# Performance work log

Hardware: AMD Instinct MI355X
Metric: run time of the kernel (lower is better)

## Reference

```python
import jax, jax.numpy as jnp
import numpy as np

NV = 20000; NC = 20000; E = 500000
IN_SHAPE = 2; PE_DIM = 8; HID = 64; NL = 3
EPS = 1e-7  # GENConv message eps


def _lin(x, w, b):
    return x @ w + b


def _encode(x, pe, ew, eb, pw1, pb1, pw2, pb2):
    # relu(cat([Linear(x), 0.5*(pe_mlp(pe)+pe_mlp(-pe))], dim=1))
    def pe_mlp(p):
        return _lin(jax.nn.relu(_lin(p, pw1, pb1)), pw2, pb2)
    h = jnp.concatenate([_lin(x, ew, eb), 0.5 * (pe_mlp(pe) + pe_mlp(-pe))], axis=1)
    return jax.nn.relu(h)


def _genconv(x_src, x_dst, src, dst, ewt, lew, leb, w1, b1, w2, b2, n_dst):
    # GENConv(aggr='softmax', t=1, norm=None, msg_norm=False, edge_dim=1)
    msg = jax.nn.relu(x_src[src] + _lin(ewt, lew, leb)) + EPS  # [E, HID]
    m = jax.ops.segment_max(msg, dst, num_segments=n_dst)      # stable segment softmax
    ex = jnp.exp(msg - m[dst])
    s = jax.ops.segment_sum(ex, dst, num_segments=n_dst)
    agg = jax.ops.segment_sum(ex / (s[dst] + 1e-16) * msg, dst, num_segments=n_dst)
    out = agg + x_dst
    return _lin(jax.nn.relu(_lin(out, w1, b1)), w2, b2)  # MLP [hid -> 2hid -> hid]


def setup_inputs() -> dict:
    key = jax.random.key(0)
    ks = iter(jax.random.split(key, 64))
    d = {}
    d['x_vals'] = jax.random.normal(next(ks), (NV, IN_SHAPE), jnp.float32)
    d['x_cons'] = jax.random.normal(next(ks), (NC, IN_SHAPE), jnp.float32)
    d['pe_vals'] = jax.random.normal(next(ks), (NV, PE_DIM), jnp.float32)
    d['pe_cons'] = jax.random.normal(next(ks), (NC, PE_DIM), jnp.float32)
    d['edge_index_v2c'] = jnp.stack([
        jax.random.randint(next(ks), (E,), 0, NV),
        jax.random.randint(next(ks), (E,), 0, NC)])
    d['edge_index_c2v'] = jnp.stack([
        jax.random.randint(next(ks), (E,), 0, NC),
        jax.random.randint(next(ks), (E,), 0, NV)])
    d['edge_weight_v2c'] = jax.random.normal(next(ks), (E, 1), jnp.float32)
    d['edge_weight_c2v'] = jax.random.normal(next(ks), (E, 1), jnp.float32)
    def p(shape):
        return jax.random.normal(next(ks), shape, jnp.float32) * 0.05
    for k_ in ['vals', 'cons']:
        d[f'enc_{k_}_w'] = p((IN_SHAPE, HID // 2)); d[f'enc_{k_}_b'] = p((HID // 2,))
        d[f'pe_{k_}_w1'] = p((PE_DIM, HID)); d[f'pe_{k_}_b1'] = p((HID,))
        d[f'pe_{k_}_w2'] = p((HID, HID // 2)); d[f'pe_{k_}_b2'] = p((HID // 2,))
    for c in ['v2c', 'c2v']:
        d[f'{c}_edge_w'] = p((NL, 1, HID)); d[f'{c}_edge_b'] = p((NL, HID))
        d[f'{c}_w1'] = p((NL, HID, 2 * HID)); d[f'{c}_b1'] = p((NL, 2 * HID))
        d[f'{c}_w2'] = p((NL, 2 * HID, HID)); d[f'{c}_b2'] = p((NL, HID))
    for k_ in ['vals', 'cons']:
        d[f'pred_{k_}_w1'] = p((HID, HID)); d[f'pred_{k_}_b1'] = p((HID,))
        d[f'pred_{k_}_w2'] = p((HID, 1)); d[f'pred_{k_}_b2'] = p((1,))
    return d


def reference(x_vals, x_cons, pe_vals, pe_cons, edge_index_v2c, edge_index_c2v,
              edge_weight_v2c, edge_weight_c2v,
              enc_vals_w, enc_vals_b, pe_vals_w1, pe_vals_b1, pe_vals_w2, pe_vals_b2,
              enc_cons_w, enc_cons_b, pe_cons_w1, pe_cons_b1, pe_cons_w2, pe_cons_b2,
              v2c_edge_w, v2c_edge_b, v2c_w1, v2c_b1, v2c_w2, v2c_b2,
              c2v_edge_w, c2v_edge_b, c2v_w1, c2v_b1, c2v_w2, c2v_b2,
              pred_vals_w1, pred_vals_b1, pred_vals_w2, pred_vals_b2,
              pred_cons_w1, pred_cons_b1, pred_cons_w2, pred_cons_b2):
    vals = _encode(x_vals, pe_vals, enc_vals_w, enc_vals_b,
                   pe_vals_w1, pe_vals_b1, pe_vals_w2, pe_vals_b2)
    cons = _encode(x_cons, pe_cons, enc_cons_w, enc_cons_b,
                   pe_cons_w1, pe_cons_b1, pe_cons_w2, pe_cons_b2)
    hv, hc = [], []
    for i in range(NL):
        cons = _genconv(vals, cons, edge_index_v2c[0], edge_index_v2c[1],
                        edge_weight_v2c, v2c_edge_w[i], v2c_edge_b[i],
                        v2c_w1[i], v2c_b1[i], v2c_w2[i], v2c_b2[i], NC)
        vals = _genconv(cons, vals, edge_index_c2v[0], edge_index_c2v[1],
                        edge_weight_c2v, c2v_edge_w[i], c2v_edge_b[i],
                        c2v_w1[i], c2v_b1[i], c2v_w2[i], c2v_b2[i], NV)
        hc.append(cons); hv.append(vals)
    V = jnp.stack(hv)  # [NL, NV, HID]
    C = jnp.stack(hc)  # [NL, NC, HID]
    pv = _lin(jax.nn.relu(_lin(V, pred_vals_w1, pred_vals_b1)), pred_vals_w2, pred_vals_b2)
    pc = _lin(jax.nn.relu(_lin(C, pred_cons_w1, pred_cons_b1)), pred_cons_w2, pred_cons_b2)
    return pv[..., 0].T, pc[..., 0].T  # [NV, NL], [NC, NL]
```

## Files before the change

### kernel.cpp

```cpp
#include <hip/hip_runtime.h>

#define NVN 20000
#define NCN 20000
#define NE  500000
#define HID 64
#define NLAYER 3
#define TN 40
#define BSH 8
#define NB 79
#define CAP 8192
#define P1E 2048

__device__ __forceinline__ float relu_(float x) { return fmaxf(x, 0.0f); }

__global__ __launch_bounds__(256) void bininit_kernel(
    int* __restrict__ bincurA, int* __restrict__ bincurB)
{
    int t = threadIdx.x;
    if (t < NB) { bincurA[t] = t * CAP; bincurB[t] = t * CAP; }
}

__global__ __launch_bounds__(256) void scatter_p1_kernel(
    const int* __restrict__ eiA, const float* __restrict__ ewA,
    int* __restrict__ bincurA, int2* __restrict__ stageA,
    const int* __restrict__ eiB, const float* __restrict__ ewB,
    int* __restrict__ bincurB, int2* __restrict__ stageB)
{
    __shared__ int rnk[P1E];
    __shared__ int cnt[NB], base_[NB];
    int t = threadIdx.x;
    int e0 = blockIdx.x * P1E;

    for (int g = 0; g < 2; ++g) {
        const int* ei   = g ? eiB : eiA;
        const float* ew = g ? ewB : ewA;
        int* bincur     = g ? bincurB : bincurA;
        int2* stage     = g ? stageB : stageA;

        if (t < NB) cnt[t] = 0;
        __syncthreads();
        for (int i = t; i < P1E; i += 256) {
            int e = e0 + i;
            if (e < NE) {
                int d = ei[NE + e];
                rnk[i] = atomicAdd(&cnt[d >> BSH], 1);
            }
        }
        __syncthreads();
        if (t < NB && cnt[t] > 0) base_[t] = atomicAdd(&bincur[t], cnt[t]);
        __syncthreads();
        for (int i = t; i < P1E; i += 256) {
            int e = e0 + i;
            if (e < NE) {
                int s = ei[e], d = ei[NE + e];
                float w = ew[e];
                stage[base_[d >> BSH] + rnk[i]] =
                    make_int2((int)((unsigned)s | ((unsigned)d << 16)), __float_as_int(w));
            }
        }
        __syncthreads();
    }
}

__global__ __launch_bounds__(1024) void scatter_p2_kernel(
    const int* __restrict__ bincurA, const int2* __restrict__ stageA,
    int* __restrict__ rowptrA, int2* __restrict__ pairA,
    const int* __restrict__ bincurB, const int2* __restrict__ stageB,
    int* __restrict__ rowptrB, int2* __restrict__ pairB)
{
    __shared__ int p[128];
    __shared__ int deg[256], pfx[256], cur[256];
    int g = blockIdx.x / NB;
    int b = blockIdx.x % NB;
    const int* bincur = g ? bincurB : bincurA;
    const int2* stage = g ? stageB : stageA;
    int* rowptr       = g ? rowptrB : rowptrA;
    int2* pair        = g ? pairB : pairA;

    int t = threadIdx.x;
    if (t < 128) p[t] = (t < NB) ? (bincur[t] - t * CAP) : 0;
    __syncthreads();
    for (int off = 1; off < 128; off <<= 1) {
        int v = (t >= off && t < 128) ? p[t - off] : 0;
        __syncthreads();
        if (t < 128) p[t] += v;
        __syncthreads();
    }
    int base = (b == 0) ? 0 : p[b - 1];
    int sz   = p[b] - base;

    int d0 = b << BSH;
    int d1 = min(d0 + 256, NCN);
    int nd = d1 - d0;
    int astart = b * CAP;

    if (t < 256) deg[t] = 0;
    __syncthreads();
    for (int e = astart + t; e < astart + sz; e += 1024) {
        int dst = (int)((unsigned)stage[e].x >> 16);
        atomicAdd(&deg[dst - d0], 1);
    }
    __syncthreads();
    if (t < 256) pfx[t] = deg[t];
    __syncthreads();
    for (int off = 1; off < 256; off <<= 1) {
        int v = (t >= off && t < 256) ? pfx[t - off] : 0;
        __syncthreads();
        if (t < 256) pfx[t] += v;
        __syncthreads();
    }
    if (t < nd) {
        int ex = base + pfx[t] - deg[t];
        rowptr[d0 + t] = ex;
        cur[t] = ex;
    }
    if (t == 0) rowptr[d1] = base + sz;
    __syncthreads();
    for (int e = astart + t; e < astart + sz; e += 1024) {
        int2 s = stage[e];
        unsigned u = (unsigned)s.x;
        int src = (int)(u & 0xFFFFu);
        int dst = (int)(u >> 16);
        int q = atomicAdd(&cur[dst - d0], 1);
        pair[q] = make_int2(src, s.y);
    }
}

__global__ __launch_bounds__(256) void encode2_kernel(
    const float* __restrict__ xv, const float* __restrict__ pev,
    const float* __restrict__ ewv, const float* __restrict__ ebv,
    const float* __restrict__ pw1v, const float* __restrict__ pb1v,
    const float* __restrict__ pw2v, const float* __restrict__ pb2v,
    const float* __restrict__ xc, const float* __restrict__ pec,
    const float* __restrict__ ewc, const float* __restrict__ ebc,
    const float* __restrict__ pw1c, const float* __restrict__ pb1c,
    const float* __restrict__ pw2c, const float* __restrict__ pb2c,
    float* __restrict__ outv, float* __restrict__ outc)
{
    __shared__ float sh[4][64];
    const int VB = (NVN + 3) / 4;
    int wave = threadIdx.x >> 6, lane = threadIdx.x & 63;
    int b = blockIdx.x;
    bool isC = (b >= VB);
    const float* x   = isC ? xc : xv;
    const float* pe  = isC ? pec : pev;
    const float* ew  = isC ? ewc : ewv;
    const float* eb  = isC ? ebc : ebv;
    const float* pw1 = isC ? pw1c : pw1v;
    const float* pb1 = isC ? pb1c : pb1v;
    const float* pw2 = isC ? pw2c : pw2v;
    const float* pb2 = isC ? pb2c : pb2v;
    float* out = isC ? outc : outv;
    int N = isC ? NCN : NVN;
    int n = (isC ? b - VB : b) * 4 + wave;
    if (n >= N) return;

    float accp = pb1[lane], accm = accp;
#pragma unroll
    for (int k = 0; k < 8; ++k) {
        float p = pe[n * 8 + k];
        float w = pw1[k * 64 + lane];
        accp += p * w;
        accm -= p * w;
    }
    float hs = 0.5f * (relu_(accp) + relu_(accm));
    float* my = sh[wave];
    my[lane] = hs;
    __builtin_amdgcn_wave_barrier();

    int col = lane & 31;
    float peo = pb2[col];
#pragma unroll
    for (int k = 0; k < 64; k += 4) {
        float4 hv = *(const float4*)(my + k);
        peo = fmaf(hv.x, pw2[(k + 0) * 32 + col], peo);
        peo = fmaf(hv.y, pw2[(k + 1) * 32 + col], peo);
        peo = fmaf(hv.z, pw2[(k + 2) * 32 + col], peo);
        peo = fmaf(hv.w, pw2[(k + 3) * 32 + col], peo);
    }
    float lino = x[n * 2 + 0] * ew[col] + x[n * 2 + 1] * ew[32 + col] + eb[col];
    float h = (lane < 32) ? lino : peo;
    out[n * 64 + lane] = relu_(h);
}

__global__ __launch_bounds__(256) void edge_agg_kernel(
    const float* __restrict__ xsrc,
    const float* __restrict__ xdst,
    const int* __restrict__ rowptr,
    const int2* __restrict__ pair,
    const float* __restrict__ lew,
    const float* __restrict__ leb,
    float* __restrict__ oa,
    int N)
{
    int wave = threadIdx.x >> 6, lane = threadIdx.x & 63;
    int n = blockIdx.x * 4 + wave;
    if (n >= N) return;

    int start = rowptr[n], end = rowptr[n + 1];
    float lw = lew[lane], lb = leb[lane];
    float xd = xdst[n * 64 + lane];

    float m0 = -1e30f, den0 = 0.0f, num0 = 0.0f;
    float m1 = -1e30f, den1 = 0.0f, num1 = 0.0f;
    int j = start;
    for (; j + 16 <= end; j += 16) {
        int idx[16]; float wv[16], msg[16];
#pragma unroll
        for (int c = 0; c < 16; ++c) {
            int2 p = pair[j + c];
            idx[c] = p.x;
            wv[c] = __int_as_float(p.y);
        }
#pragma unroll
        for (int c = 0; c < 16; ++c) {
            float xv = xsrc[idx[c] * 64 + lane];
            msg[c] = relu_(fmaf(wv[c], lw, xv + lb)) + 1e-7f;
        }
        {
            float a0 = fmaxf(msg[0], msg[1]), a1 = fmaxf(msg[2], msg[3]);
            float a2 = fmaxf(msg[4], msg[5]), a3 = fmaxf(msg[6], msg[7]);
            float mnew = fmaxf(m0, fmaxf(fmaxf(a0, a1), fmaxf(a2, a3)));
            float sc = __expf(m0 - mnew);
            float cd = 0.0f, cn = 0.0f;
#pragma unroll
            for (int c = 0; c < 8; ++c) {
                float e = __expf(msg[c] - mnew);
                cd += e;
                cn = fmaf(e, msg[c], cn);
            }
            den0 = fmaf(den0, sc, cd);
            num0 = fmaf(num0, sc, cn);
            m0 = mnew;
        }
        {
            float a0 = fmaxf(msg[8], msg[9]), a1 = fmaxf(msg[10], msg[11]);
            float a2 = fmaxf(msg[12], msg[13]), a3 = fmaxf(msg[14], msg[15]);
            float mnew = fmaxf(m1, fmaxf(fmaxf(a0, a1), fmaxf(a2, a3)));
            float sc = __expf(m1 - mnew);
            float cd = 0.0f, cn = 0.0f;
#pragma unroll
            for (int c = 8; c < 16; ++c) {
                float e = __expf(msg[c] - mnew);
                cd += e;
                cn = fmaf(e, msg[c], cn);
            }
            den1 = fmaf(den1, sc, cd);
            num1 = fmaf(num1, sc, cn);
            m1 = mnew;
        }
    }
    if (j < end) {
        int last = end - 1;
        int idx[16]; float wv[16], msg[16]; bool val[16];
#pragma unroll
        for (int c = 0; c < 16; ++c) {
            int jj = j + c;
            val[c] = jj < end;
            int jc = val[c] ? jj : last;
            int2 p = pair[jc];
            idx[c] = p.x;
            wv[c] = __int_as_float(p.y);
        }
#pragma unroll
        for (int c = 0; c < 16; ++c) {
            float xv = xsrc[idx[c] * 64 + lane];
            float tm = relu_(fmaf(wv[c], lw, xv + lb)) + 1e-7f;
            msg[c] = val[c] ? tm : -1e30f;
        }
        {
            float a0 = fmaxf(msg[0], msg[1]), a1 = fmaxf(msg[2], msg[3]);
            float a2 = fmaxf(msg[4], msg[5]), a3 = fmaxf(msg[6], msg[7]);
            float mnew = fmaxf(m0, fmaxf(fmaxf(a0, a1), fmaxf(a2, a3)));
            float sc = __expf(m0 - mnew);
            float cd = 0.0f, cn = 0.0f;
#pragma unroll
            for (int c = 0; c < 8; ++c) {
                float e = __expf(msg[c] - mnew);
                cd += e;
                cn = fmaf(e, msg[c], cn);
            }
            den0 = fmaf(den0, sc, cd);
            num0 = fmaf(num0, sc, cn);
            m0 = mnew;
        }
        {
            float a0 = fmaxf(msg[8], msg[9]), a1 = fmaxf(msg[10], msg[11]);
            float a2 = fmaxf(msg[12], msg[13]), a3 = fmaxf(msg[14], msg[15]);
            float mnew = fmaxf(m1, fmaxf(fmaxf(a0, a1), fmaxf(a2, a3)));
            float sc = __expf(m1 - mnew);
            float cd = 0.0f, cn = 0.0f;
#pragma unroll
            for (int c = 8; c < 16; ++c) {
                float e = __expf(msg[c] - mnew);
                cd += e;
                cn = fmaf(e, msg[c], cn);
            }
            den1 = fmaf(den1, sc, cd);
            num1 = fmaf(num1, sc, cn);
            m1 = mnew;
        }
    }
    float M = fmaxf(m0, m1);
    float s0 = __expf(m0 - M), s1 = __expf(m1 - M);
    float den = den0 * s0 + den1 * s1;
    float num = num0 * s0 + num1 * s1;

    oa[n * 64 + lane] = num / (den + 1e-16f) + xd;
}

__global__ __launch_bounds__(256) void mlp_kernel(
    const float* __restrict__ oa,
    float* __restrict__ feat,
    const float* __restrict__ w1,
    const float* __restrict__ b1,
    const float* __restrict__ w2,
    const float* __restrict__ b2,
    const float* __restrict__ pw1,
    const float* __restrict__ pb1,
    const float* __restrict__ pw2,
    const float* __restrict__ pb2,
    float* __restrict__ outp,
    int N, int layer)
{
    __shared__ float w1s[64 * 128];
    __shared__ float w2s[128 * 64];
    __shared__ float pw1s[64 * 64];
    __shared__ float b1s[128];
    __shared__ float b2s[64];
    __shared__ float pb1s[64];
    __shared__ float pw2s[64];
    __shared__ float act[TN][68];
    __shared__ float hid[TN][132];

    int tid = threadIdx.x;
    for (int i = tid; i < 64 * 128; i += 256) w1s[i] = w1[i];
    for (int i = tid; i < 128 * 64; i += 256) w2s[i] = w2[i];
    for (int i = tid; i < 64 * 64; i += 256) pw1s[i] = pw1[i];
    if (tid < 128) b1s[tid] = b1[tid];
    if (tid < 64) { b2s[tid] = b2[tid]; pb1s[tid] = pb1[tid]; pw2s[tid] = pw2[tid]; }
    float pb2v = pb2[0];

    int o4 = (tid & 31) * 4;
    int o2 = (tid & 31) * 2;
    int n5 = (tid >> 5) * 5;
    __syncthreads();

    int ntiles = N / TN;
    for (int tile = blockIdx.x; tile < ntiles; tile += gridDim.x) {
        int base = tile * TN;
        {
            const float* g = oa + (size_t)base * 64;
            for (int i = tid; i < TN * 64; i += 256)
                act[i >> 6][i & 63] = g[i];
        }
        __syncthreads();

        {
            float acc[5][4];
#pragma unroll
            for (int i = 0; i < 5; ++i)
#pragma unroll
                for (int q = 0; q < 4; ++q) acc[i][q] = b1s[o4 + q];
            for (int k = 0; k < 64; k += 4) {
                float4 a[5];
#pragma unroll
                for (int i = 0; i < 5; ++i) a[i] = *(const float4*)&act[n5 + i][k];
                float4 w0 = *(const float4*)&w1s[(k + 0) * 128 + o4];
                float4 wq1 = *(const float4*)&w1s[(k + 1) * 128 + o4];
                float4 wq2 = *(const float4*)&w1s[(k + 2) * 128 + o4];
                float4 wq3 = *(const float4*)&w1s[(k + 3) * 128 + o4];
#pragma unroll
                for (int i = 0; i < 5; ++i) {
                    acc[i][0] = fmaf(a[i].x, w0.x, acc[i][0]);
                    acc[i][1] = fmaf(a[i].x, w0.y, acc[i][1]);
                    acc[i][2] = fmaf(a[i].x, w0.z, acc[i][2]);
                    acc[i][3] = fmaf(a[i].x, w0.w, acc[i][3]);
                    acc[i][0] = fmaf(a[i].y, wq1.x, acc[i][0]);
                    acc[i][1] = fmaf(a[i].y, wq1.y, acc[i][1]);
                    acc[i][2] = fmaf(a[i].y, wq1.z, acc[i][2]);
                    acc[i][3] = fmaf(a[i].y, wq1.w, acc[i][3]);
                    acc[i][0] = fmaf(a[i].z, wq2.x, acc[i][0]);
                    acc[i][1] = fmaf(a[i].z, wq2.y, acc[i][1]);
                    acc[i][2] = fmaf(a[i].z, wq2.z, acc[i][2]);
                    acc[i][3] = fmaf(a[i].z, wq2.w, acc[i][3]);
                    acc[i][0] = fmaf(a[i].w, wq3.x, acc[i][0]);
                    acc[i][1] = fmaf(a[i].w, wq3.y, acc[i][1]);
                    acc[i][2] = fmaf(a[i].w, wq3.z, acc[i][2]);
                    acc[i][3] = fmaf(a[i].w, wq3.w, acc[i][3]);
                }
            }
#pragma unroll
            for (int i = 0; i < 5; ++i) {
                float4 h4 = make_float4(relu_(acc[i][0]), relu_(acc[i][1]),
                                        relu_(acc[i][2]), relu_(acc[i][3]));
                *(float4*)&hid[n5 + i][o4] = h4;
            }
        }
        __syncthreads();

        {
            float acc[5][2];
#pragma unroll
            for (int i = 0; i < 5; ++i) { acc[i][0] = b2s[o2]; acc[i][1] = b2s[o2 + 1]; }
            for (int k = 0; k < 128; k += 4) {
                float4 a[5];
#pragma unroll
                for (int i = 0; i < 5; ++i) a[i] = *(const float4*)&hid[n5 + i][k];
                float2 w0 = *(const float2*)&w2s[(k + 0) * 64 + o2];
                float2 wq1 = *(const float2*)&w2s[(k + 1) * 64 + o2];
                float2 wq2 = *(const float2*)&w2s[(k + 2) * 64 + o2];
                float2 wq3 = *(const float2*)&w2s[(k + 3) * 64 + o2];
#pragma unroll
                for (int i = 0; i < 5; ++i) {
                    acc[i][0] = fmaf(a[i].x, w0.x, acc[i][0]);
                    acc[i][1] = fmaf(a[i].x, w0.y, acc[i][1]);
                    acc[i][0] = fmaf(a[i].y, wq1.x, acc[i][0]);
                    acc[i][1] = fmaf(a[i].y, wq1.y, acc[i][1]);
                    acc[i][0] = fmaf(a[i].z, wq2.x, acc[i][0]);
                    acc[i][1] = fmaf(a[i].z, wq2.y, acc[i][1]);
                    acc[i][0] = fmaf(a[i].w, wq3.x, acc[i][0]);
                    acc[i][1] = fmaf(a[i].w, wq3.y, acc[i][1]);
                }
            }
#pragma unroll
            for (int i = 0; i < 5; ++i) {
                float2 r2 = make_float2(acc[i][0], acc[i][1]);
                *(float2*)&feat[(size_t)(base + n5 + i) * 64 + o2] = r2;
                *(float2*)&act[n5 + i][o2] = r2;
            }
        }
        __syncthreads();

        {
            float acc[5][2];
#pragma unroll
            for (int i = 0; i < 5; ++i) { acc[i][0] = pb1s[o2]; acc[i][1] = pb1s[o2 + 1]; }
            for (int k = 0; k < 64; k += 4) {
                float4 a[5];
#pragma unroll
                for (int i = 0; i < 5; ++i) a[i] = *(const float4*)&act[n5 + i][k];
                float2 w0 = *(const float2*)&pw1s[(k + 0) * 64 + o2];
                float2 wq1 = *(const float2*)&pw1s[(k + 1) * 64 + o2];
                float2 wq2 = *(const float2*)&pw1s[(k + 2) * 64 + o2];
                float2 wq3 = *(const float2*)&pw1s[(k + 3) * 64 + o2];
#pragma unroll
                for (int i = 0; i < 5; ++i) {
                    acc[i][0] = fmaf(a[i].x, w0.x, acc[i][0]);
                    acc[i][1] = fmaf(a[i].x, w0.y, acc[i][1]);
                    acc[i][0] = fmaf(a[i].y, wq1.x, acc[i][0]);
                    acc[i][1] = fmaf(a[i].y, wq1.y, acc[i][1]);
                    acc[i][0] = fmaf(a[i].z, wq2.x, acc[i][0]);
                    acc[i][1] = fmaf(a[i].z, wq2.y, acc[i][1]);
                    acc[i][0] = fmaf(a[i].w, wq3.x, acc[i][0]);
                    acc[i][1] = fmaf(a[i].w, wq3.y, acc[i][1]);
                }
            }
            float pw2a = pw2s[o2], pw2b = pw2s[o2 + 1];
            float ps[5];
#pragma unroll
            for (int i = 0; i < 5; ++i)
                ps[i] = relu_(acc[i][0]) * pw2a + relu_(acc[i][1]) * pw2b;
#pragma unroll
            for (int msk = 16; msk >= 1; msk >>= 1) {
#pragma unroll
                for (int i = 0; i < 5; ++i)
                    ps[i] += __shfl_xor(ps[i], msk, 64);
            }
            if ((tid & 31) == 0) {
#pragma unroll
                for (int i = 0; i < 5; ++i)
                    outp[(size_t)(base + n5 + i) * NLAYER + layer] = ps[i] + pb2v;
            }
        }
        __syncthreads();
    }
}

extern "C" void kernel_launch(void* const* d_in, const int* in_sizes, int n_in,
                              void* d_out, int out_size, void* d_ws, size_t ws_size,
                              hipStream_t stream)
{
    const float* x_vals   = (const float*)d_in[0];
    const float* x_cons   = (const float*)d_in[1];
    const float* pe_vals  = (const float*)d_in[2];
    const float* pe_cons  = (const float*)d_in[3];
    const int*   ei_v2c   = (const int*)d_in[4];
    const int*   ei_c2v   = (const int*)d_in[5];
    const float* ew_v2c   = (const float*)d_in[6];
    const float* ew_c2v   = (const float*)d_in[7];
    const float* enc_vals_w = (const float*)d_in[8];
    const float* enc_vals_b = (const float*)d_in[9];
    const float* pe_vals_w1 = (const float*)d_in[10];
    const float* pe_vals_b1 = (const float*)d_in[11];
    const float* pe_vals_w2 = (const float*)d_in[12];
    const float* pe_vals_b2 = (const float*)d_in[13];
    const float* enc_cons_w = (const float*)d_in[14];
    const float* enc_cons_b = (const float*)d_in[15];
    const float* pe_cons_w1 = (const float*)d_in[16];
    const float* pe_cons_b1 = (const float*)d_in[17];
    const float* pe_cons_w2 = (const float*)d_in[18];
    const float* pe_cons_b2 = (const float*)d_in[19];
    const float* v2c_edge_w = (const float*)d_in[20];
    const float* v2c_edge_b = (const float*)d_in[21];
    const float* v2c_w1     = (const float*)d_in[22];
    const float* v2c_b1     = (const float*)d_in[23];
    const float* v2c_w2     = (const float*)d_in[24];
    const float* v2c_b2     = (const float*)d_in[25];
    const float* c2v_edge_w = (const float*)d_in[26];
    const float* c2v_edge_b = (const float*)d_in[27];
    const float* c2v_w1     = (const float*)d_in[28];
    const float* c2v_b1     = (const float*)d_in[29];
    const float* c2v_w2     = (const float*)d_in[30];
    const float* c2v_b2     = (const float*)d_in[31];
    const float* pred_vals_w1 = (const float*)d_in[32];
    const float* pred_vals_b1 = (const float*)d_in[33];
    const float* pred_vals_w2 = (const float*)d_in[34];
    const float* pred_vals_b2 = (const float*)d_in[35];
    const float* pred_cons_w1 = (const float*)d_in[36];
    const float* pred_cons_b1 = (const float*)d_in[37];
    const float* pred_cons_w2 = (const float*)d_in[38];
    const float* pred_cons_b2 = (const float*)d_in[39];

    float* out = (float*)d_out;
    float* out_c = out + (size_t)NVN * NLAYER;

    const size_t NF = (size_t)NVN * 64;
    const size_t ARENA = (size_t)NB * CAP;

    float* ws     = (float*)d_ws;
    float* feat_v = ws;
    float* feat_c = feat_v + NF;
    float* oa     = feat_c + NF;
    int2* v2c_pair  = (int2*)(oa + NF);
    int2* c2v_pair  = v2c_pair + NE;
    int2* v2c_stage = c2v_pair + NE;
    int2* c2v_stage = v2c_stage + ARENA;
    int* ip = (int*)(c2v_stage + ARENA);
    int* v2c_bincur  = ip; ip += NB;
    int* c2v_bincur  = ip; ip += NB;
    int* v2c_rowptr  = ip; ip += NCN + 1;
    int* c2v_rowptr  = ip; ip += NVN + 1;

    const int p1b = (NE + P1E - 1) / P1E;

    bininit_kernel<<<1, 256, 0, stream>>>(v2c_bincur, c2v_bincur);
    scatter_p1_kernel<<<p1b, 256, 0, stream>>>(
        ei_v2c, ew_v2c, v2c_bincur, v2c_stage,
        ei_c2v, ew_c2v, c2v_bincur, c2v_stage);
    scatter_p2_kernel<<<2 * NB, 1024, 0, stream>>>(
        v2c_bincur, v2c_stage, v2c_rowptr, v2c_pair,
        c2v_bincur, c2v_stage, c2v_rowptr, c2v_pair);

    encode2_kernel<<<(NVN + 3) / 4 + (NCN + 3) / 4, 256, 0, stream>>>(
        x_vals, pe_vals, enc_vals_w, enc_vals_b,
        pe_vals_w1, pe_vals_b1, pe_vals_w2, pe_vals_b2,
        x_cons, pe_cons, enc_cons_w, enc_cons_b,
        pe_cons_w1, pe_cons_b1, pe_cons_w2, pe_cons_b2,
        feat_v, feat_c);

    for (int i = 0; i < NLAYER; ++i) {
        edge_agg_kernel<<<(NCN + 3) / 4, 256, 0, stream>>>(
            feat_v, feat_c, v2c_rowptr, v2c_pair,
            v2c_edge_w + (size_t)i * HID, v2c_edge_b + (size_t)i * HID,
            oa, NCN);
        mlp_kernel<<<250, 256, 0, stream>>>(
            oa, feat_c,
            v2c_w1 + (size_t)i * 8192, v2c_b1 + (size_t)i * 128,
            v2c_w2 + (size_t)i * 8192, v2c_b2 + (size_t)i * 64,
            pred_cons_w1, pred_cons_b1, pred_cons_w2, pred_cons_b2,
            out_c, NCN, i);
        edge_agg_kernel<<<(NVN + 3) / 4, 256, 0, stream>>>(
            feat_c, feat_v, c2v_rowptr, c2v_pair,
            c2v_edge_w + (size_t)i * HID, c2v_edge_b + (size_t)i * HID,
            oa, NVN);
        mlp_kernel<<<250, 256, 0, stream>>>(
            oa, feat_v,
            c2v_w1 + (size_t)i * 8192, c2v_b1 + (size_t)i * 128,
            c2v_w2 + (size_t)i * 8192, c2v_b2 + (size_t)i * 64,
            pred_vals_w1, pred_vals_b1, pred_vals_w2, pred_vals_b2,
            out, NVN, i);
    }
}
```

Measured before the change: 515.8 us.

## Split node features into two 32-column halves and gather half-rows per block

Node feature tables are stored as two planar halves of 32 columns each (offset NF2). The edge aggregation kernel now launches twice as many blocks, one per half. Within a wave, the two 32-lane halves process alternate groups of 16 edges, and their softmax partials are combined with a cross-lane shuffle. Edge pair loads and the output store use nontemporal hints. The goal is 128-byte gathers that improve cache locality per half-table, at the cost of reading the edge list twice and leaving half the lanes idle on the store.

```diff
diff --git a/kernel.cpp b/kernel.cpp
--- a/kernel.cpp
+++ b/kernel.cpp
@@ -10,6 +10,7 @@
 #define NB 79
 #define CAP 8192
 #define P1E 2048
+#define NF2 640000
 
 __device__ __forceinline__ float relu_(float x) { return fmaxf(x, 0.0f); }
 
@@ -180,7 +181,7 @@
     }
     float lino = x[n * 2 + 0] * ew[col] + x[n * 2 + 1] * ew[32 + col] + eb[col];
     float h = (lane < 32) ? lino : peo;
-    out[n * 64 + lane] = relu_(h);
+    out[(size_t)(lane >> 5) * NF2 + (size_t)n * 32 + (lane & 31)] = relu_(h);
 }
 
 __global__ __launch_bounds__(256) void edge_agg_kernel(
@@ -194,119 +195,101 @@
     int N)
 {
     int wave = threadIdx.x >> 6, lane = threadIdx.x & 63;
-    int n = blockIdx.x * 4 + wave;
+    int h = blockIdx.x & 1;
+    int n = (blockIdx.x >> 1) * 4 + wave;
     if (n >= N) return;
-
+    int eh = lane >> 5;
+    int c  = lane & 31;
+
+    const float* tab = xsrc + (size_t)h * NF2;
     int start = rowptr[n], end = rowptr[n + 1];
-    float lw = lew[lane], lb = leb[lane];
-    float xd = xdst[n * 64 + lane];
-
-    float m0 = -1e30f, den0 = 0.0f, num0 = 0.0f;
-    float m1 = -1e30f, den1 = 0.0f, num1 = 0.0f;
+    float lw = lew[h * 32 + c], lb = leb[h * 32 + c];
+    float xd = xdst[(size_t)h * NF2 + (size_t)n * 32 + c];
+
+    float m = -1e30f, den = 0.0f, num = 0.0f;
+    int off = eh * 16;
     int j = start;
-    for (; j + 16 <= end; j += 16) {
+    for (; j + 32 <= end; j += 32) {
         int idx[16]; float wv[16], msg[16];
 #pragma unroll
-        for (int c = 0; c < 16; ++c) {
-            int2 p = pair[j + c];
-            idx[c] = p.x;
-            wv[c] = __int_as_float(p.y);
-        }
-#pragma unroll
-        for (int c = 0; c < 16; ++c) {
-            float xv = xsrc[idx[c] * 64 + lane];
-            msg[c] = relu_(fmaf(wv[c], lw, xv + lb)) + 1e-7f;
-        }
-        {
-            float a0 = fmaxf(msg[0], msg[1]), a1 = fmaxf(msg[2], msg[3]);
-            float a2 = fmaxf(msg[4], msg[5]), a3 = fmaxf(msg[6], msg[7]);
-            float mnew = fmaxf(m0, fmaxf(fmaxf(a0, a1), fmaxf(a2, a3)));
-            float sc = __expf(m0 - mnew);
-            float cd = 0.0f, cn = 0.0f;
-#pragma unroll
-            for (int c = 0; c < 8; ++c) {
-                float e = __expf(msg[c] - mnew);
-                cd += e;
-                cn = fmaf(e, msg[c], cn);
-            }
-            den0 = fmaf(den0, sc, cd);
-            num0 = fmaf(num0, sc, cn);
-            m0 = mnew;
-        }
-        {
-            float a0 = fmaxf(msg[8], msg[9]), a1 = fmaxf(msg[10], msg[11]);
-            float a2 = fmaxf(msg[12], msg[13]), a3 = fmaxf(msg[14], msg[15]);
-            float mnew = fmaxf(m1, fmaxf(fmaxf(a0, a1), fmaxf(a2, a3)));
-            float sc = __expf(m1 - mnew);
-            float cd = 0.0f, cn = 0.0f;
-#pragma unroll
-            for (int c = 8; c < 16; ++c) {
-                float e = __expf(msg[c] - mnew);
-                cd += e;
-                cn = fmaf(e, msg[c], cn);
-            }
-            den1 = fmaf(den1, sc, cd);
-            num1 = fmaf(num1, sc, cn);
-            m1 = mnew;
-        }
+        for (int s = 0; s < 16; ++s) {
+            long long pv = __builtin_nontemporal_load(
+                (const long long*)(pair + (j + off + s)));
+            idx[s] = (int)pv;
+            wv[s] = __int_as_float((int)(pv >> 32));
+        }
+#pragma unroll
+        for (int s = 0; s < 16; ++s) {
+            float xv = tab[idx[s] * 32 + c];
+            msg[s] = relu_(fmaf(wv[s], lw, xv + lb)) + 1e-7f;
+        }
+        float a0 = fmaxf(msg[0], msg[1]), a1 = fmaxf(msg[2], msg[3]);
+        float a2 = fmaxf(msg[4], msg[5]), a3 = fmaxf(msg[6], msg[7]);
+        float a4 = fmaxf(msg[8], msg[9]), a5 = fmaxf(msg[10], msg[11]);
+        float a6 = fmaxf(msg[12], msg[13]), a7 = fmaxf(msg[14], msg[15]);
+        float b0 = fmaxf(fmaxf(a0, a1), fmaxf(a2, a3));
+        float b1 = fmaxf(fmaxf(a4, a5), fmaxf(a6, a7));
+        float mnew = fmaxf(m, fmaxf(b0, b1));
+        float sc = __expf(m - mnew);
+        float cd = 0.0f, cn = 0.0f;
+#pragma unroll
+        for (int s = 0; s < 16; ++s) {
+            float e = __expf(msg[s] - mnew);
+            cd += e;
+            cn = fmaf(e, msg[s], cn);
+        }
+        den = fmaf(den, sc, cd);
+        num = fmaf(num, sc, cn);
+        m = mnew;
     }
     if (j < end) {
         int last = end - 1;
         int idx[16]; float wv[16], msg[16]; bool val[16];
 #pragma unroll
-        for (int c = 0; c < 16; ++c) {
-            int jj = j + c;
-            val[c] = jj < end;
-            int jc = val[c] ? jj : last;
-            int2 p = pair[jc];
-            idx[c] = p.x;
-            wv[c] = __int_as_float(p.y);
-        }
-#pragma unroll
-        for (int c = 0; c < 16; ++c) {
-            float xv = xsrc[idx[c] * 64 + lane];
-            float tm = relu_(fmaf(wv[c], lw, xv + lb)) + 1e-7f;
-            msg[c] = val[c] ? tm : -1e30f;
-        }
-        {
-            float a0 = fmaxf(msg[0], msg[1]), a1 = fmaxf(msg[2], msg[3]);
-            float a2 = fmaxf(msg[4], msg[5]), a3 = fmaxf(msg[6], msg[7]);
-            float mnew = fmaxf(m0, fmaxf(fmaxf(a0, a1), fmaxf(a2, a3)));
-            float sc = __expf(m0 - mnew);
-            float cd = 0.0f, cn = 0.0f;
-#pragma unroll
-            for (int c = 0; c < 8; ++c) {
-                float e = __expf(msg[c] - mnew);
-                cd += e;
-                cn = fmaf(e, msg[c], cn);
-            }
-            den0 = fmaf(den0, sc, cd);
-            num0 = fmaf(num0, sc, cn);
-            m0 = mnew;
-        }
-        {
-            float a0 = fmaxf(msg[8], msg[9]), a1 = fmaxf(msg[10], msg[11]);
-            float a2 = fmaxf(msg[12], msg[13]), a3 = fmaxf(msg[14], msg[15]);
-            float mnew = fmaxf(m1, fmaxf(fmaxf(a0, a1), fmaxf(a2, a3)));
-            float sc = __expf(m1 - mnew);
-            float cd = 0.0f, cn = 0.0f;
-#pragma unroll
-            for (int c = 8; c < 16; ++c) {
-                float e = __expf(msg[c] - mnew);
-                cd += e;
-                cn = fmaf(e, msg[c], cn);
-            }
-            den1 = fmaf(den1, sc, cd);
-            num1 = fmaf(num1, sc, cn);
-            m1 = mnew;
-        }
-    }
-    float M = fmaxf(m0, m1);
-    float s0 = __expf(m0 - M), s1 = __expf(m1 - M);
-    float den = den0 * s0 + den1 * s1;
-    float num = num0 * s0 + num1 * s1;
-
-    oa[n * 64 + lane] = num / (den + 1e-16f) + xd;
+        for (int s = 0; s < 16; ++s) {
+            int jj = j + off + s;
+            val[s] = jj < end;
+            int jc = val[s] ? jj : last;
+            long long pv = __builtin_nontemporal_load(
+                (const long long*)(pair + jc));
+            idx[s] = (int)pv;
+            wv[s] = __int_as_float((int)(pv >> 32));
+        }
+#pragma unroll
+        for (int s = 0; s < 16; ++s) {
+            float xv = tab[idx[s] * 32 + c];
+            float tm = relu_(fmaf(wv[s], lw, xv + lb)) + 1e-7f;
+            msg[s] = val[s] ? tm : -1e30f;
+        }
+        float a0 = fmaxf(msg[0], msg[1]), a1 = fmaxf(msg[2], msg[3]);
+        float a2 = fmaxf(msg[4], msg[5]), a3 = fmaxf(msg[6], msg[7]);
+        float a4 = fmaxf(msg[8], msg[9]), a5 = fmaxf(msg[10], msg[11]);
+        float a6 = fmaxf(msg[12], msg[13]), a7 = fmaxf(msg[14], msg[15]);
+        float b0 = fmaxf(fmaxf(a0, a1), fmaxf(a2, a3));
+        float b1 = fmaxf(fmaxf(a4, a5), fmaxf(a6, a7));
+        float mnew = fmaxf(m, fmaxf(b0, b1));
+        float sc = __expf(m - mnew);
+        float cd = 0.0f, cn = 0.0f;
+#pragma unroll
+        for (int s = 0; s < 16; ++s) {
+            float e = __expf(msg[s] - mnew);
+            cd += e;
+            cn = fmaf(e, msg[s], cn);
+        }
+        den = fmaf(den, sc, cd);
+        num = fmaf(num, sc, cn);
+        m = mnew;
+    }
+    float mo  = __shfl_xor(m, 32, 64);
+    float dho = __shfl_xor(den, 32, 64);
+    float nho = __shfl_xor(num, 32, 64);
+    float M = fmaxf(m, mo);
+    float s0 = __expf(m - M), s1 = __expf(mo - M);
+    float DEN = fmaf(den, s0, dho * s1);
+    float NUM = fmaf(num, s0, nho * s1);
+    float o = NUM / (DEN + 1e-16f) + xd;
+    if (lane < 32)
+        __builtin_nontemporal_store(o, oa + (size_t)n * 64 + h * 32 + lane);
 }
 
 __global__ __launch_bounds__(256) void mlp_kernel(
@@ -344,6 +327,8 @@
     int o4 = (tid & 31) * 4;
     int o2 = (tid & 31) * 2;
     int n5 = (tid >> 5) * 5;
+    int oh = o2 >> 5;
+    int oc = o2 & 31;
     __syncthreads();
 
     int ntiles = N / TN;
@@ -426,7 +411,7 @@
 #pragma unroll
             for (int i = 0; i < 5; ++i) {
                 float2 r2 = make_float2(acc[i][0], acc[i][1]);
-                *(float2*)&feat[(size_t)(base + n5 + i) * 64 + o2] = r2;
+                *(float2*)&feat[(size_t)oh * NF2 + (size_t)(base + n5 + i) * 32 + oc] = r2;
                 *(float2*)&act[n5 + i][o2] = r2;
             }
         }
@@ -559,8 +544,11 @@
         pe_cons_w1, pe_cons_b1, pe_cons_w2, pe_cons_b2,
         feat_v, feat_c);
 
+    const int eag_v = 2 * ((NVN + 3) / 4);
+    const int eag_c = 2 * ((NCN + 3) / 4);
+
     for (int i = 0; i < NLAYER; ++i) {
-        edge_agg_kernel<<<(NCN + 3) / 4, 256, 0, stream>>>(
+        edge_agg_kernel<<<eag_c, 256, 0, stream>>>(
             feat_v, feat_c, v2c_rowptr, v2c_pair,
             v2c_edge_w + (size_t)i * HID, v2c_edge_b + (size_t)i * HID,
             oa, NCN);
@@ -570,7 +558,7 @@
             v2c_w2 + (size_t)i * 8192, v2c_b2 + (size_t)i * 64,
             pred_cons_w1, pred_cons_b1, pred_cons_w2, pred_cons_b2,
             out_c, NCN, i);
-        edge_agg_kernel<<<(NVN + 3) / 4, 256, 0, stream>>>(
+        edge_agg_kernel<<<eag_v, 256, 0, stream>>>(
             feat_c, feat_v, c2v_rowptr, c2v_pair,
             c2v_edge_w + (size_t)i * HID, c2v_edge_b + (size_t)i * HID,
             oa, NVN);
```

Measured after the change: 598.8 us. 16.1% more time.
